# Kernel optimization log

Hardware: AMD Instinct MI355X
Metric: run time of the kernel (lower is better)

The kernel has to match this reference:

```python
import jax, jax.numpy as jnp
import numpy as np

L = 401            # cfg.n_anchor_bins
MIN_SEP = 2        # cfg.min_separation_bins
TARGET_ALPHA = 0.85
DIST_W, CTCF_W, COMP_W = 1.0, 0.5, 0.5
RATIO_TARGET = 1.5


def setup_inputs() -> dict:
    key = jax.random.key(0)
    k1, k2, k3 = jax.random.split(key, 3)
    B = 256
    contact_map = jax.random.normal(k1, (B, L, L), dtype=jnp.float32)
    compartment_logits = jax.random.normal(k2, (B, L, 2), dtype=jnp.float32)
    ctcf_orientation = (jax.random.randint(k3, (B, L), 0, 3) - 1).astype(jnp.int32)  # {-1,0,1}
    return {"contact_map": contact_map,
            "compartment_logits": compartment_logits,
            "ctcf_orientation": ctcf_orientation}


def reference(contact_map, compartment_logits, ctcf_orientation):
    B, Ld, _ = contact_map.shape
    dt = contact_map.dtype
    idx = jnp.arange(Ld)
    d = jnp.abs(idx[:, None] - idx[None, :])          # (L, L) int distance bins

    # ---- distance decay loss: one segment-reduce instead of a loop over bins ----
    bins = d.reshape(-1)                               # (L*L,)
    cm_sum = contact_map.sum(0).reshape(-1)            # sum over batch, flattened
    per_bin_sum = jax.ops.segment_sum(cm_sum, bins, num_segments=Ld)
    counts = jax.ops.segment_sum(jnp.ones_like(cm_sum), bins, num_segments=Ld)
    mean_c = per_bin_sum / (counts * B)                # mean contact per distance s
    s_vals = jnp.arange(Ld).astype(dt)
    valid = (idx >= MIN_SEP) & jnp.isfinite(mean_c) & (mean_c > 0)
    w = valid.astype(dt)
    n = w.sum()
    log_d = jnp.log(jnp.maximum(s_vals, 1.0))
    log_p = jnp.log(jnp.where(valid, mean_c, 1.0) + 1e-6)
    n_safe = jnp.maximum(n, 1.0)
    x_mean = (w * log_d).sum() / n_safe
    y_mean = (w * log_p).sum() / n_safe
    num = (w * (log_d - x_mean) * (log_p - y_mean)).sum()
    den = (w * (log_d - x_mean) ** 2).sum() + 1e-8
    slope = num / den
    dist_loss = jnp.where(n >= 5, (slope + TARGET_ALPHA) ** 2, jnp.zeros((), dt))

    # ---- CTCF convergence loss ----
    f = (ctcf_orientation == 1).astype(dt)             # (B, L)
    r = (ctcf_orientation == -1).astype(dt)
    convergent = f[:, :, None] * r[:, None, :]         # (B, L, L)
    any_c = (ctcf_orientation != 0).astype(dt)
    any_pair = any_c[:, :, None] * any_c[:, None, :]
    non_conv = any_pair * (1.0 - convergent)
    nc_sum = non_conv.sum()
    hinge = (jax.nn.relu(contact_map) * non_conv).sum() / (nc_sum + 1e-6)
    ctcf_loss = jnp.where(nc_sum < 1.0, jnp.zeros((), dt), hinge)

    # ---- compartment loss ----
    comp = jnp.argmax(jax.lax.stop_gradient(compartment_logits), axis=-1)  # (B, L)
    same = (comp[:, :, None] == comp[:, None, :]).astype(dt)               # (B, L, L)
    maskf = (d >= MIN_SEP).astype(dt)[None]                                # (1, L, L)
    within = (contact_map * same * maskf).sum() / jnp.maximum((same * maskf).sum(), 1.0)
    between = (contact_map * (1.0 - same) * maskf).sum() / jnp.maximum(((1.0 - same) * maskf).sum(), 1.0)
    ratio = within / (jnp.abs(between) + 1e-6)
    comp_loss = jax.nn.relu(RATIO_TARGET - ratio)

    total = DIST_W * dist_loss + CTCF_W * ctcf_loss + COMP_W * comp_loss
    return jnp.stack([dist_loss, ctcf_loss, comp_loss, total])
```

## Files before the change

kernel.cpp:

```cpp
#include <hip/hip_runtime.h>
#include <cmath>

#define LBINS 401
#define LL 160801
#define MIN_SEP 2
#define PSTRIDE 405
#define UNR 8

#define ACC_HANY  401
#define ACC_HCONV 402
#define ACC_SWM   403
#define ACC_SMM   404
#define ACCD_OFF  416
#define PARTS_OFF 512

__global__ void zero_kernel(double* __restrict__ accd) {
    if (threadIdx.x < 2) accd[threadIdx.x] = 0.0;
}

__global__ __launch_bounds__(128)
void prep_kernel(const float* __restrict__ logits,
                 const int* __restrict__ ctcf,
                 double* __restrict__ accd) {
    int b = blockIdx.x;
    int tid = threadIdx.x;
    int n1 = 0, nf = 0, nr = 0, na = 0, adj = 0;
    const float* lg = logits + (size_t)b * LBINS * 2;
    const int*   ct = ctcf   + (size_t)b * LBINS;
    for (int l = tid; l < LBINS; l += 128) {
        int o = ct[l];
        int ci = (lg[2 * l + 1] > lg[2 * l]) ? 1 : 0;
        n1 += ci; nf += (o == 1); nr += (o == -1); na += (o != 0);
        if (l >= 1) {
            int cp = (lg[2 * (l - 1) + 1] > lg[2 * (l - 1)]) ? 1 : 0;
            adj += (ci == cp);
        }
    }
    #pragma unroll
    for (int off = 32; off > 0; off >>= 1) {
        n1 += __shfl_down(n1, off, 64);
        nf += __shfl_down(nf, off, 64);
        nr += __shfl_down(nr, off, 64);
        na += __shfl_down(na, off, 64);
        adj += __shfl_down(adj, off, 64);
    }
    __shared__ int ired[2][5];
    int w = tid >> 6;
    if ((tid & 63) == 0) {
        ired[w][0] = n1; ired[w][1] = nf; ired[w][2] = nr;
        ired[w][3] = na; ired[w][4] = adj;
    }
    __syncthreads();
    if (tid == 0) {
        int N1 = ired[0][0] + ired[1][0];
        int NF = ired[0][1] + ired[1][1];
        int NR = ired[0][2] + ired[1][2];
        int NA = ired[0][3] + ired[1][3];
        int AD = ired[0][4] + ired[1][4];
        int N0 = LBINS - N1;
        unsafeAtomicAdd(&accd[0], (double)NA * NA - (double)NF * NR);
        unsafeAtomicAdd(&accd[1],
            (double)N0 * N0 + (double)N1 * N1 - (double)LBINS - 2.0 * AD);
    }
}

__global__ __launch_bounds__(256)
void diag_kernel(const float* __restrict__ cm,
                 const float* __restrict__ logits,
                 const int* __restrict__ ctcf,
                 float* __restrict__ parts) {
    int b      = blockIdx.x;
    int ihalf  = blockIdx.y & 1;
    int kgroup = blockIdx.y >> 1;
    int u      = threadIdx.x;
    int k      = kgroup * 256 + u;
    bool active = (k < LBINS);

    __shared__ float4 colm[LBINS];
    __shared__ float4 rowm[LBINS];
    __shared__ float  lb[LBINS];
    __shared__ float  sred[4][4];

    const int*   ct = ctcf   + (size_t)b * LBINS;
    const float* lg = logits + (size_t)b * LBINS * 2;
    for (int t = u; t < LBINS; t += 256) {
        int o = ct[t];
        float any = (o != 0) ? 1.f : 0.f;
        float rev = (o == -1) ? 1.f : 0.f;
        float fwd = (o == 1) ? 1.f : 0.f;
        float cj  = (lg[2 * t + 1] > lg[2 * t]) ? 1.f : 0.f;
        colm[t] = make_float4(any, rev, cj, 0.f);
        rowm[t] = make_float4(any, fwd, 2.f * cj - 1.f, 1.f - cj);
        lb[t] = 0.f;
    }
    __syncthreads();

    int i0 = ihalf ? 201 : 0;
    int ie = ihalf ? LBINS : 201;

    const float* cmb = cm + (size_t)b * LL;
    float HA = 0.f, HC = 0.f;
    float SMk = 0.f, SMw = 0.f, SWk = 0.f, SWw = 0.f;

    if (active) {
        int i = i0;
        for (; i + UNR <= ie; i += UNR) {
            float  cv[UNR], sw[UNR];
            float4 cj4[UNR], rm4[UNR];
            #pragma unroll
            for (int q = 0; q < UNR; ++q) {
                int ii = i + q;
                int j  = ii + k;
                int wrapped = (j >= LBINS);
                int jc = wrapped ? j - LBINS : j;
                cv[q]  = cmb[(size_t)ii * LBINS + jc];
                cj4[q] = colm[jc];
                rm4[q] = rowm[ii];
                sw[q]  = wrapped ? 1.f : 0.f;
            }
            #pragma unroll
            for (int q = 0; q < UNR; ++q) {
                float c  = cv[q];
                float rc = fmaxf(c, 0.f);
                HA = fmaf(rm4[q].x * cj4[q].x, rc, HA);
                HC = fmaf(rm4[q].y * cj4[q].y, rc, HC);
                float same = fmaf(rm4[q].z, cj4[q].z, rm4[q].w);
                float sc = same * c;
                float s = sw[q];
                SWw = fmaf(s, sc, SWw);
                SWk = fmaf(1.f - s, sc, SWk);
                SMw = fmaf(s, c, SMw);
                SMk = fmaf(1.f - s, c, SMk);
            }
        }
        for (; i < ie; ++i) {
            int j  = i + k;
            int wrapped = (j >= LBINS);
            int jc = wrapped ? j - LBINS : j;
            float c = cmb[(size_t)i * LBINS + jc];
            float4 cjv = colm[jc];
            float4 rm  = rowm[i];
            float s = wrapped ? 1.f : 0.f;
            float rc = fmaxf(c, 0.f);
            HA = fmaf(rm.x * cjv.x, rc, HA);
            HC = fmaf(rm.y * cjv.y, rc, HC);
            float same = fmaf(rm.z, cjv.z, rm.w);
            float sc = same * c;
            SWw = fmaf(s, sc, SWw);
            SWk = fmaf(1.f - s, sc, SWk);
            SMw = fmaf(s, c, SMw);
            SMk = fmaf(1.f - s, c, SMk);
        }
    }

    float SWm = 0.f, SMm = 0.f;
    if (active) {
        int dw = LBINS - k;
        atomicAdd(&lb[k], SMk);
        if (k > 0) atomicAdd(&lb[dw], SMw);
        float mk = (k >= MIN_SEP) ? 1.f : 0.f;
        float mw = (dw >= MIN_SEP) ? 1.f : 0.f;
        SWm = SWk * mk + SWw * mw;
        SMm = SMk * mk + SMw * mw;
    }

    #pragma unroll
    for (int off = 32; off > 0; off >>= 1) {
        HA  += __shfl_down(HA,  off, 64);
        HC  += __shfl_down(HC,  off, 64);
        SWm += __shfl_down(SWm, off, 64);
        SMm += __shfl_down(SMm, off, 64);
    }
    int w = u >> 6;
    if ((u & 63) == 0) {
        sred[w][0] = HA; sred[w][1] = HC; sred[w][2] = SWm; sred[w][3] = SMm;
    }
    __syncthreads();

    float* pout = parts + (size_t)(blockIdx.y * gridDim.x + blockIdx.x) * PSTRIDE;
    for (int t = u; t < LBINS; t += 256) pout[t] = lb[t];
    if (u == 0) {
        float a = 0.f, c2 = 0.f, s = 0.f, m = 0.f;
        #pragma unroll
        for (int q = 0; q < 4; ++q) {
            a += sred[q][0]; c2 += sred[q][1]; s += sred[q][2]; m += sred[q][3];
        }
        pout[401] = a; pout[402] = c2; pout[403] = s; pout[404] = m;
    }
}

__global__ __launch_bounds__(256)
void reduce_kernel(const float* __restrict__ parts,
                   float* __restrict__ accum, int npart) {
    int s = blockIdx.x;
    int u = threadIdx.x;
    float acc = 0.f;
    for (int p = u; p < npart; p += 256) acc += parts[(size_t)p * PSTRIDE + s];
    #pragma unroll
    for (int off = 32; off > 0; off >>= 1) acc += __shfl_down(acc, off, 64);
    __shared__ float r[4];
    if ((u & 63) == 0) r[u >> 6] = acc;
    __syncthreads();
    if (u == 0) accum[s] = r[0] + r[1] + r[2] + r[3];
}

__device__ double block_reduce_d(double v, double* buf) {
    int tid = threadIdx.x;
    buf[tid] = v;
    __syncthreads();
    for (int off = blockDim.x >> 1; off > 0; off >>= 1) {
        if (tid < off) buf[tid] += buf[tid + off];
        __syncthreads();
    }
    double r = buf[0];
    __syncthreads();
    return r;
}

__global__ __launch_bounds__(512)
void final_kernel(const float* __restrict__ accum,
                  const double* __restrict__ accd,
                  float* __restrict__ out, int B) {
    __shared__ double dred[512];
    int tid = threadIdx.x;

    double nc_sum   = accd[0];
    double same_cnt = accd[1];
    double total_maskf = (double)B * ((double)LL - 3.0 * LBINS + 2.0);
    double diff_cnt = total_maskf - same_cnt;

    float wgt = 0.f, x = 0.f, y = 0.f;
    if (tid < LBINS) {
        float cntB = ((tid == 0) ? (float)LBINS : 2.0f * (float)(LBINS - tid)) * (float)B;
        float mc = accum[tid] / cntB;
        int valid = (tid >= MIN_SEP) && __builtin_isfinite(mc) && (mc > 0.0f);
        wgt = valid ? 1.f : 0.f;
        x = logf(fmaxf((float)tid, 1.0f));
        y = logf((valid ? mc : 1.0f) + 1e-6f);
    }
    double n  = block_reduce_d((double)wgt, dred);
    double Sx = block_reduce_d((double)wgt * x, dred);
    double Sy = block_reduce_d((double)wgt * y, dred);
    double n_safe = fmax(n, 1.0);
    double xm = Sx / n_safe, ym = Sy / n_safe;
    double num = block_reduce_d((double)wgt * ((double)x - xm) * ((double)y - ym), dred);
    double den = block_reduce_d((double)wgt * ((double)x - xm) * ((double)x - xm), dred);

    if (tid == 0) {
        double slope = num / (den + 1e-8);
        float dist_loss = (n >= 5.0) ? (float)((slope + 0.85) * (slope + 0.85)) : 0.0f;

        float ncf = (float)nc_sum;
        float hinge = (accum[ACC_HANY] - accum[ACC_HCONV]) / (ncf + 1e-6f);
        float ctcf_loss = (ncf < 1.0f) ? 0.0f : hinge;

        float SW_m = accum[ACC_SWM];
        float SM_m = accum[ACC_SMM];
        float within  = SW_m / (float)fmax(same_cnt, 1.0);
        float between = (SM_m - SW_m) / (float)fmax(diff_cnt, 1.0);
        float ratio = within / (fabsf(between) + 1e-6f);
        float comp_loss = fmaxf(1.5f - ratio, 0.0f);

        float total = 1.0f * dist_loss + 0.5f * ctcf_loss + 0.5f * comp_loss;
        out[0] = dist_loss;
        out[1] = ctcf_loss;
        out[2] = comp_loss;
        out[3] = total;
    }
}

extern "C" void kernel_launch(void* const* d_in, const int* in_sizes, int n_in,
                              void* d_out, int out_size, void* d_ws, size_t ws_size,
                              hipStream_t stream) {
    const float* cm     = (const float*)d_in[0];
    const float* logits = (const float*)d_in[1];
    const int*   ctcf   = (const int*)d_in[2];
    float* out = (float*)d_out;

    int total = in_sizes[0];
    int B = total / LL;

    float*  wsf   = (float*)d_ws;
    float*  accum = wsf;
    double* accd  = (double*)(wsf + ACCD_OFF);
    float*  parts = wsf + PARTS_OFF;
    int npart = 4 * B;

    zero_kernel<<<1, 64, 0, stream>>>(accd);
    prep_kernel<<<B, 128, 0, stream>>>(logits, ctcf, accd);
    diag_kernel<<<dim3(B, 4), 256, 0, stream>>>(cm, logits, ctcf, parts);
    reduce_kernel<<<PSTRIDE, 256, 0, stream>>>(parts, accum, npart);
    final_kernel<<<1, 512, 0, stream>>>(accum, accd, out, B);
}
```

Baseline: 256.3 us.

## Fuse prep counts into diag kernel and split rows into quarters

Removes the zero and prep launches. The per-batch CTCF and compartment count products are now computed inside the diagonal kernel by the first row-quarter block, written per batch as floats, and reduced in the final kernel, so double atomics are no longer needed. The diagonal work is re-split into four row quarters per batch, and each thread handles diagonal u and, when it exists, 256+u. This avoids the mostly idle second k-group blocks, but threads below 145 now process two diagonals one after the other.

```diff
diff --git a/kernel.cpp b/kernel.cpp
--- a/kernel.cpp
+++ b/kernel.cpp
@@ -11,56 +11,60 @@
 #define ACC_HCONV 402
 #define ACC_SWM   403
 #define ACC_SMM   404
-#define ACCD_OFF  416
-#define PARTS_OFF 512
-
-__global__ void zero_kernel(double* __restrict__ accd) {
-    if (threadIdx.x < 2) accd[threadIdx.x] = 0.0;
-}
-
-__global__ __launch_bounds__(128)
-void prep_kernel(const float* __restrict__ logits,
-                 const int* __restrict__ ctcf,
-                 double* __restrict__ accd) {
-    int b = blockIdx.x;
-    int tid = threadIdx.x;
-    int n1 = 0, nf = 0, nr = 0, na = 0, adj = 0;
-    const float* lg = logits + (size_t)b * LBINS * 2;
-    const int*   ct = ctcf   + (size_t)b * LBINS;
-    for (int l = tid; l < LBINS; l += 128) {
-        int o = ct[l];
-        int ci = (lg[2 * l + 1] > lg[2 * l]) ? 1 : 0;
-        n1 += ci; nf += (o == 1); nr += (o == -1); na += (o != 0);
-        if (l >= 1) {
-            int cp = (lg[2 * (l - 1) + 1] > lg[2 * (l - 1)]) ? 1 : 0;
-            adj += (ci == cp);
-        }
-    }
-    #pragma unroll
-    for (int off = 32; off > 0; off >>= 1) {
-        n1 += __shfl_down(n1, off, 64);
-        nf += __shfl_down(nf, off, 64);
-        nr += __shfl_down(nr, off, 64);
-        na += __shfl_down(na, off, 64);
-        adj += __shfl_down(adj, off, 64);
-    }
-    __shared__ int ired[2][5];
-    int w = tid >> 6;
-    if ((tid & 63) == 0) {
-        ired[w][0] = n1; ired[w][1] = nf; ired[w][2] = nr;
-        ired[w][3] = na; ired[w][4] = adj;
-    }
-    __syncthreads();
-    if (tid == 0) {
-        int N1 = ired[0][0] + ired[1][0];
-        int NF = ired[0][1] + ired[1][1];
-        int NR = ired[0][2] + ired[1][2];
-        int NA = ired[0][3] + ired[1][3];
-        int AD = ired[0][4] + ired[1][4];
-        int N0 = LBINS - N1;
-        unsafeAtomicAdd(&accd[0], (double)NA * NA - (double)NF * NR);
-        unsafeAtomicAdd(&accd[1],
-            (double)N0 * N0 + (double)N1 * N1 - (double)LBINS - 2.0 * AD);
+#define CNT_OFF   512
+#define PARTS_OFF 2048
+
+__device__ __forceinline__ void run_diag(
+    const float* __restrict__ cmb, const float4* colm, const float4* rowm,
+    int k, int i0, int ie,
+    float& HA, float& HC, float& SMk, float& SMw, float& SWk, float& SWw) {
+    int i = i0;
+    for (; i + UNR <= ie; i += UNR) {
+        float  cv[UNR], sw[UNR];
+        float4 cj4[UNR], rm4[UNR];
+        #pragma unroll
+        for (int q = 0; q < UNR; ++q) {
+            int ii = i + q;
+            int j  = ii + k;
+            int wrapped = (j >= LBINS);
+            int jc = wrapped ? j - LBINS : j;
+            cv[q]  = cmb[(size_t)ii * LBINS + jc];
+            cj4[q] = colm[jc];
+            rm4[q] = rowm[ii];
+            sw[q]  = wrapped ? 1.f : 0.f;
+        }
+        #pragma unroll
+        for (int q = 0; q < UNR; ++q) {
+            float c  = cv[q];
+            float rc = fmaxf(c, 0.f);
+            HA = fmaf(rm4[q].x * cj4[q].x, rc, HA);
+            HC = fmaf(rm4[q].y * cj4[q].y, rc, HC);
+            float same = fmaf(rm4[q].z, cj4[q].z, rm4[q].w);
+            float sc = same * c;
+            float s = sw[q];
+            SWw = fmaf(s, sc, SWw);
+            SWk = fmaf(1.f - s, sc, SWk);
+            SMw = fmaf(s, c, SMw);
+            SMk = fmaf(1.f - s, c, SMk);
+        }
+    }
+    for (; i < ie; ++i) {
+        int j  = i + k;
+        int wrapped = (j >= LBINS);
+        int jc = wrapped ? j - LBINS : j;
+        float c = cmb[(size_t)i * LBINS + jc];
+        float4 cjv = colm[jc];
+        float4 rm  = rowm[i];
+        float s = wrapped ? 1.f : 0.f;
+        float rc = fmaxf(c, 0.f);
+        HA = fmaf(rm.x * cjv.x, rc, HA);
+        HC = fmaf(rm.y * cjv.y, rc, HC);
+        float same = fmaf(rm.z, cjv.z, rm.w);
+        float sc = same * c;
+        SWw = fmaf(s, sc, SWw);
+        SWk = fmaf(1.f - s, sc, SWk);
+        SMw = fmaf(s, c, SMw);
+        SMk = fmaf(1.f - s, c, SMk);
     }
 }
 
@@ -68,18 +72,17 @@
 void diag_kernel(const float* __restrict__ cm,
                  const float* __restrict__ logits,
                  const int* __restrict__ ctcf,
+                 float* __restrict__ cnt,
                  float* __restrict__ parts) {
-    int b      = blockIdx.x;
-    int ihalf  = blockIdx.y & 1;
-    int kgroup = blockIdx.y >> 1;
-    int u      = threadIdx.x;
-    int k      = kgroup * 256 + u;
-    bool active = (k < LBINS);
+    int b = blockIdx.x;
+    int qr = blockIdx.y;
+    int u = threadIdx.x;
 
     __shared__ float4 colm[LBINS];
     __shared__ float4 rowm[LBINS];
     __shared__ float  lb[LBINS];
     __shared__ float  sred[4][4];
+    __shared__ float  cred[4][5];
 
     const int*   ct = ctcf   + (size_t)b * LBINS;
     const float* lg = logits + (size_t)b * LBINS * 2;
@@ -95,73 +98,68 @@
     }
     __syncthreads();
 
-    int i0 = ihalf ? 201 : 0;
-    int ie = ihalf ? LBINS : 201;
-
+    if (qr == 0) {
+        float n1 = 0.f, nf = 0.f, nr = 0.f, na = 0.f, adj = 0.f;
+        for (int t = u; t < LBINS; t += 256) {
+            float4 cv = colm[t];
+            n1 += cv.z; na += cv.x; nr += cv.y;
+            nf += rowm[t].y;
+            if (t >= 1) adj += (colm[t - 1].z == cv.z) ? 1.f : 0.f;
+        }
+        #pragma unroll
+        for (int off = 32; off > 0; off >>= 1) {
+            n1 += __shfl_down(n1, off, 64);
+            nf += __shfl_down(nf, off, 64);
+            nr += __shfl_down(nr, off, 64);
+            na += __shfl_down(na, off, 64);
+            adj += __shfl_down(adj, off, 64);
+        }
+        int w = u >> 6;
+        if ((u & 63) == 0) {
+            cred[w][0] = n1; cred[w][1] = nf; cred[w][2] = nr;
+            cred[w][3] = na; cred[w][4] = adj;
+        }
+        __syncthreads();
+        if (u == 0) {
+            float N1 = 0.f, NF = 0.f, NR = 0.f, NA = 0.f, AD = 0.f;
+            #pragma unroll
+            for (int q = 0; q < 4; ++q) {
+                N1 += cred[q][0]; NF += cred[q][1]; NR += cred[q][2];
+                NA += cred[q][3]; AD += cred[q][4];
+            }
+            float N0 = (float)LBINS - N1;
+            cnt[2 * b]     = NA * NA - NF * NR;
+            cnt[2 * b + 1] = N0 * N0 + N1 * N1 - (float)LBINS - 2.f * AD;
+        }
+    }
+
+    int i0 = (qr * LBINS) >> 2;
+    int ie = ((qr + 1) * LBINS) >> 2;
     const float* cmb = cm + (size_t)b * LL;
-    float HA = 0.f, HC = 0.f;
-    float SMk = 0.f, SMw = 0.f, SWk = 0.f, SWw = 0.f;
-
-    if (active) {
-        int i = i0;
-        for (; i + UNR <= ie; i += UNR) {
-            float  cv[UNR], sw[UNR];
-            float4 cj4[UNR], rm4[UNR];
-            #pragma unroll
-            for (int q = 0; q < UNR; ++q) {
-                int ii = i + q;
-                int j  = ii + k;
-                int wrapped = (j >= LBINS);
-                int jc = wrapped ? j - LBINS : j;
-                cv[q]  = cmb[(size_t)ii * LBINS + jc];
-                cj4[q] = colm[jc];
-                rm4[q] = rowm[ii];
-                sw[q]  = wrapped ? 1.f : 0.f;
-            }
-            #pragma unroll
-            for (int q = 0; q < UNR; ++q) {
-                float c  = cv[q];
-                float rc = fmaxf(c, 0.f);
-                HA = fmaf(rm4[q].x * cj4[q].x, rc, HA);
-                HC = fmaf(rm4[q].y * cj4[q].y, rc, HC);
-                float same = fmaf(rm4[q].z, cj4[q].z, rm4[q].w);
-                float sc = same * c;
-                float s = sw[q];
-                SWw = fmaf(s, sc, SWw);
-                SWk = fmaf(1.f - s, sc, SWk);
-                SMw = fmaf(s, c, SMw);
-                SMk = fmaf(1.f - s, c, SMk);
-            }
-        }
-        for (; i < ie; ++i) {
-            int j  = i + k;
-            int wrapped = (j >= LBINS);
-            int jc = wrapped ? j - LBINS : j;
-            float c = cmb[(size_t)i * LBINS + jc];
-            float4 cjv = colm[jc];
-            float4 rm  = rowm[i];
-            float s = wrapped ? 1.f : 0.f;
-            float rc = fmaxf(c, 0.f);
-            HA = fmaf(rm.x * cjv.x, rc, HA);
-            HC = fmaf(rm.y * cjv.y, rc, HC);
-            float same = fmaf(rm.z, cjv.z, rm.w);
-            float sc = same * c;
-            SWw = fmaf(s, sc, SWw);
-            SWk = fmaf(1.f - s, sc, SWk);
-            SMw = fmaf(s, c, SMw);
-            SMk = fmaf(1.f - s, c, SMk);
-        }
-    }
-
-    float SWm = 0.f, SMm = 0.f;
-    if (active) {
+
+    float HA = 0.f, HC = 0.f, SWm = 0.f, SMm = 0.f;
+
+    {
+        int k = u;
+        float SMk = 0.f, SMw = 0.f, SWk = 0.f, SWw = 0.f;
+        run_diag(cmb, colm, rowm, k, i0, ie, HA, HC, SMk, SMw, SWk, SWw);
         int dw = LBINS - k;
         atomicAdd(&lb[k], SMk);
         if (k > 0) atomicAdd(&lb[dw], SMw);
         float mk = (k >= MIN_SEP) ? 1.f : 0.f;
         float mw = (dw >= MIN_SEP) ? 1.f : 0.f;
-        SWm = SWk * mk + SWw * mw;
-        SMm = SMk * mk + SMw * mw;
+        SWm += SWk * mk + SWw * mw;
+        SMm += SMk * mk + SMw * mw;
+    }
+    if (u < LBINS - 256) {
+        int k = 256 + u;
+        float SMk = 0.f, SMw = 0.f, SWk = 0.f, SWw = 0.f;
+        run_diag(cmb, colm, rowm, k, i0, ie, HA, HC, SMk, SMw, SWk, SWw);
+        int dw = LBINS - k;
+        atomicAdd(&lb[k], SMk);
+        atomicAdd(&lb[dw], SMw);
+        SWm += SWk + SWw;
+        SMm += SMk + SMw;
     }
 
     #pragma unroll
@@ -177,7 +175,7 @@
     }
     __syncthreads();
 
-    float* pout = parts + (size_t)(blockIdx.y * gridDim.x + blockIdx.x) * PSTRIDE;
+    float* pout = parts + (size_t)(qr * gridDim.x + b) * PSTRIDE;
     for (int t = u; t < LBINS; t += 256) pout[t] = lb[t];
     if (u == 0) {
         float a = 0.f, c2 = 0.f, s = 0.f, m = 0.f;
@@ -219,13 +217,18 @@
 
 __global__ __launch_bounds__(512)
 void final_kernel(const float* __restrict__ accum,
-                  const double* __restrict__ accd,
+                  const float* __restrict__ cnt,
                   float* __restrict__ out, int B) {
     __shared__ double dred[512];
     int tid = threadIdx.x;
 
-    double nc_sum   = accd[0];
-    double same_cnt = accd[1];
+    double ncl = 0.0, samel = 0.0;
+    for (int p = tid; p < B; p += 512) {
+        ncl   += (double)cnt[2 * p];
+        samel += (double)cnt[2 * p + 1];
+    }
+    double nc_sum   = block_reduce_d(ncl, dred);
+    double same_cnt = block_reduce_d(samel, dred);
     double total_maskf = (double)B * ((double)LL - 3.0 * LBINS + 2.0);
     double diff_cnt = total_maskf - same_cnt;
 
@@ -280,15 +283,12 @@
     int total = in_sizes[0];
     int B = total / LL;
 
-    float*  wsf   = (float*)d_ws;
-    float*  accum = wsf;
-    double* accd  = (double*)(wsf + ACCD_OFF);
-    float*  parts = wsf + PARTS_OFF;
-    int npart = 4 * B;
-
-    zero_kernel<<<1, 64, 0, stream>>>(accd);
-    prep_kernel<<<B, 128, 0, stream>>>(logits, ctcf, accd);
-    diag_kernel<<<dim3(B, 4), 256, 0, stream>>>(cm, logits, ctcf, parts);
-    reduce_kernel<<<PSTRIDE, 256, 0, stream>>>(parts, accum, npart);
-    final_kernel<<<1, 512, 0, stream>>>(accum, accd, out, B);
-}
+    float* wsf   = (float*)d_ws;
+    float* accum = wsf;
+    float* cnt   = wsf + CNT_OFF;
+    float* parts = wsf + PARTS_OFF;
+
+    diag_kernel<<<dim3(B, 4), 256, 0, stream>>>(cm, logits, ctcf, cnt, parts);
+    reduce_kernel<<<PSTRIDE, 256, 0, stream>>>(parts, accum, 4 * B);
+    final_kernel<<<1, 512, 0, stream>>>(accum, cnt, out, B);
+}
```

New measurement: 284.4 us. 1.11x slower.
